# Performance work log

Hardware: AMD Instinct MI355X
Metric: run time of the kernel (lower is better)

The kernel has to match this reference:

```python
import jax, jax.numpy as jnp
import numpy as np

DIM = 1024
HEADS = 16
DIM_HEAD = 64
INNER = HEADS * DIM_HEAD
B, M, N = 8, 4096, 256
EPS = 1e-5


def layer_norm(x, g, b):
    mu = jnp.mean(x, axis=-1, keepdims=True)
    var = jnp.mean(jnp.square(x - mu), axis=-1, keepdims=True)
    return (x - mu) * jax.lax.rsqrt(var + EPS) * g + b


def setup_inputs() -> dict:
    key = jax.random.key(0)
    ks = jax.random.split(key, 8)
    x = jax.random.normal(ks[0], (B, M, DIM), dtype=jnp.float32)
    latents = jax.random.normal(ks[1], (B, N, DIM), dtype=jnp.float32)
    x_att_mask = jax.random.randint(ks[2], (B, M), 0, 2) == 1  # True = masked
    s = 0.02
    Wq = jax.random.normal(ks[3], (DIM, INNER), dtype=jnp.float32) * s
    Wkv = jax.random.normal(ks[4], (DIM, 2 * INNER), dtype=jnp.float32) * s
    Wo = jax.random.normal(ks[5], (INNER, DIM), dtype=jnp.float32) * s
    return {
        "x": x, "latents": latents, "x_att_mask": x_att_mask,
        "nm_g": jnp.ones((DIM,), jnp.float32), "nm_b": jnp.zeros((DIM,), jnp.float32),
        "nl_g": jnp.ones((DIM,), jnp.float32), "nl_b": jnp.zeros((DIM,), jnp.float32),
        "Wq": Wq, "Wkv": Wkv, "Wo": Wo,
    }


def reference(x, latents, x_att_mask, nm_g, nm_b, nl_g, nl_b, Wq, Wkv, Wo):
    b, n, d = latents.shape
    h, dh = HEADS, DIM_HEAD
    scale = dh ** (-0.5)

    # additive mask: concat(media mask, all-False latent mask); True -> -inf, False -> +1 (faithful quirk)
    latent_mask = jnp.zeros((b, n), dtype=bool)
    full_mask = jnp.concatenate([x_att_mask, latent_mask], axis=1)  # [b, m+n]
    add_mask = jnp.where(full_mask, -jnp.inf, 1.0).astype(x.dtype)[:, None, None, :]  # [b,1,1,m+n]

    xn = layer_norm(x, nm_g, nm_b)
    ln = layer_norm(latents, nl_g, nl_b)

    q = (ln @ Wq).reshape(b, n, h, dh).transpose(0, 2, 1, 3)  # bhnd
    kv_in = jnp.concatenate([xn, ln], axis=1)                 # [b, m+n, d]
    kv = kv_in @ Wkv
    k, v = jnp.split(kv, 2, axis=-1)
    j = kv_in.shape[1]
    k = k.reshape(b, j, h, dh).transpose(0, 2, 1, 3)
    v = v.reshape(b, j, h, dh).transpose(0, 2, 1, 3)

    sim = jnp.einsum('bhid,bhjd->bhij', q * scale, k)
    sim = sim - jnp.max(sim, axis=-1, keepdims=True)
    sim = sim + add_mask
    attn = jax.nn.softmax(sim, axis=-1)
    out = jnp.einsum('bhij,bhjd->bhid', attn, v)
    out = out.transpose(0, 2, 1, 3).reshape(b, n, h * dh)
    return out @ Wo
```

## Files before the change

kernel.cpp:

```cpp
#include <hip/hip_runtime.h>
#include <hip/hip_bf16.h>
#include <stdint.h>

#define HEADS 16
#define DH    64
#define NB    8
#define MQ    256
#define MX    4096
#define JD    4352
#define DIMV  1024
#define GK    1024

typedef __bf16 bf16;
typedef __bf16 bf16x8 __attribute__((ext_vector_type(8)));
typedef float  f32x4  __attribute__((ext_vector_type(4)));

#define SWZ(r, c) (((c) ^ ((r) & 7)))

#define VMW(n) asm volatile("s_waitcnt vmcnt(" #n ")" ::: "memory")

__device__ __forceinline__ void gl_lds16(const void* g, void* l) {
  __builtin_amdgcn_global_load_lds((const __attribute__((address_space(1))) void*)g,
                                   (__attribute__((address_space(3))) void*)l, 16, 0, 0);
}

__global__ __launch_bounds__(256) void ln_kernel(
    const float* __restrict__ X, const float* __restrict__ gw, const float* __restrict__ bw,
    bf16* __restrict__ out_kv, bf16* __restrict__ out_ln, int is_lat)
{
  const int row = blockIdx.x;
  const int tid = threadIdx.x;
  const float4 v = ((const float4*)(X + (size_t)row * DIMV))[tid];
  float s  = v.x + v.y + v.z + v.w;
  float s2 = v.x*v.x + v.y*v.y + v.z*v.z + v.w*v.w;
#pragma unroll
  for (int m = 1; m < 64; m <<= 1) { s += __shfl_xor(s, m); s2 += __shfl_xor(s2, m); }
  __shared__ float red[8];
  const int wid = tid >> 6;
  if ((tid & 63) == 0) { red[wid*2] = s; red[wid*2+1] = s2; }
  __syncthreads();
  s  = red[0] + red[2] + red[4] + red[6];
  s2 = red[1] + red[3] + red[5] + red[7];
  const float mu  = s * (1.0f / DIMV);
  const float var = s2 * (1.0f / DIMV) - mu * mu;
  const float rst = rsqrtf(var + 1e-5f);
  const float4 g4 = ((const float4*)gw)[tid];
  const float4 b4 = ((const float4*)bw)[tid];
  union { bf16 h[4]; short4 s4; } u;
  u.h[0] = (bf16)((v.x - mu) * rst * g4.x + b4.x);
  u.h[1] = (bf16)((v.y - mu) * rst * g4.y + b4.y);
  u.h[2] = (bf16)((v.z - mu) * rst * g4.z + b4.z);
  u.h[3] = (bf16)((v.w - mu) * rst * g4.w + b4.w);
  size_t kvrow;
  if (is_lat) { int b = row >> 8;  int i = row & 255;  kvrow = (size_t)b * JD + MX + i; }
  else        { int b = row >> 12; int j = row & 4095; kvrow = (size_t)b * JD + j; }
  *(short4*)(out_kv + kvrow * DIMV + tid * 4) = u.s4;
  if (is_lat) *(short4*)(out_ln + (size_t)row * DIMV + tid * 4) = u.s4;
}

__global__ __launch_bounds__(256) void transpose_w(
    const float* __restrict__ in, bf16* __restrict__ out, int R, int C)
{
  __shared__ float t[64][65];
  const int tilesC = C >> 6;
  const int tc = blockIdx.x % tilesC, tr = blockIdx.x / tilesC;
  const int r0 = tr << 6, c0 = tc << 6;
  const int lr = threadIdx.x >> 4;
  const int lc = (threadIdx.x & 15) << 2;
#pragma unroll
  for (int p = 0; p < 4; p++) {
    float4 v = *(const float4*)&in[(size_t)(r0 + lr + p*16) * C + c0 + lc];
    t[lr + p*16][lc    ] = v.x; t[lr + p*16][lc + 1] = v.y;
    t[lr + p*16][lc + 2] = v.z; t[lr + p*16][lc + 3] = v.w;
  }
  __syncthreads();
#pragma unroll
  for (int p = 0; p < 4; p++) {
    const int oc = lr + p*16;
    union { bf16 h[4]; short4 s4; } u;
    u.h[0] = (bf16)t[lc    ][oc]; u.h[1] = (bf16)t[lc + 1][oc];
    u.h[2] = (bf16)t[lc + 2][oc]; u.h[3] = (bf16)t[lc + 3][oc];
    *(short4*)&out[(size_t)(c0 + oc) * R + r0 + lc] = u.s4;
  }
}

__global__ __launch_bounds__(256) void mask_detect(
    const unsigned char* __restrict__ m, int n, int* __restrict__ flag)
{
  const int tid = threadIdx.x;
  int cnt = 0;
  for (int i = tid; i < n; i += 256) cnt += (m[i] != 0) ? 1 : 0;
#pragma unroll
  for (int mm = 1; mm < 64; mm <<= 1) cnt += __shfl_xor(cnt, mm);
  __shared__ int r4[4];
  if ((tid & 63) == 0) r4[tid >> 6] = cnt;
  __syncthreads();
  if (tid == 0) {
    int t = r4[0] + r4[1] + r4[2] + r4[3];
    flag[0] = (t * 16 > n * 5) ? 1 : 0;
  }
}

__global__ __launch_bounds__(256) void mask_build(
    const void* __restrict__ mraw, const int* __restrict__ flag, float* __restrict__ madd)
{
  const int idx = blockIdx.x * 256 + threadIdx.x;
  const int b = idx / JD, j = idx - b * JD;
  float v = 0.0f;
  if (j < MX) {
    bool masked = (*flag) ? (((const unsigned char*)mraw)[b * MX + j] != 0)
                          : (((const int*)mraw)[b * MX + j] != 0);
    v = masked ? -20000.0f : 0.0f;
  }
  madd[idx] = v;
}

__global__ __launch_bounds__(512, 2) void gemm256(
    const bf16* __restrict__ A, const bf16* __restrict__ Bt,
    const bf16* __restrict__ Aq, const bf16* __restrict__ Bq,
    bf16* __restrict__ outR, bf16* __restrict__ outVT, bf16* __restrict__ outQ)
{
  __shared__ bf16 sm[65536];

  const int tid = threadIdx.x;
  const int lane = tid & 63, wid = tid >> 6;
  const int wr = wid >> 2, wc = wid & 3;
  const int lc = lane & 15, lq = lane >> 4;
  const int srow = tid >> 3, sc = tid & 7;
  const int ssw = SWZ(srow, sc) * 8;

  int bid = blockIdx.x;
  bid = (bid & 7) * 140 + (bid >> 3);

  const bf16 *Arow, *Brow;
  int m0, n0, omode;
  if (bid < 1088) {
    const int by = bid >> 3, bx = bid & 7;
    m0 = by * 256;
    if (bx < 4) { n0 = bx * 256;
      Arow = A  + (size_t)m0 * GK; Brow = Bt + (size_t)n0 * GK; omode = 0; }
    else        { n0 = 1024 + (bx - 4) * 256;
      Arow = Bt + (size_t)n0 * GK; Brow = A  + (size_t)m0 * GK; omode = 1; }
  } else {
    const int ix = bid - 1088;
    m0 = (ix >> 2) * 256; n0 = (ix & 3) * 256;
    Arow = Aq + (size_t)m0 * GK; Brow = Bq + (size_t)n0 * GK; omode = 2;
  }

  const bf16* Abase = Arow + (size_t)srow * GK + ssw;
  const bf16* Bbase = Brow + (size_t)srow * GK + ssw;

  auto stA = [&](int d, int h, int kt) {
#pragma unroll
    for (int l = 0; l < 2; ++l)
      gl_lds16(Abase + (size_t)(h*128 + l*64) * GK + kt * 64,
               &sm[d*32768 + (h*128 + l*64)*64 + tid*8]);
  };
  auto stB = [&](int d, int h, int kt) {
#pragma unroll
    for (int l = 0; l < 2; ++l)
      gl_lds16(Bbase + (size_t)(h*128 + l*64) * GK + kt * 64,
               &sm[d*32768 + 16384 + (h*128 + l*64)*64 + tid*8]);
  };

  f32x4 acc[8][4];
#pragma unroll
  for (int i = 0; i < 8; i++)
#pragma unroll
    for (int j = 0; j < 4; j++)
#pragma unroll
      for (int r = 0; r < 4; r++) acc[i][j][r] = 0.f;

#define DS_PHASE(d, q, STAGE_STMT, WAIT_STMT)                                  \
  {                                                                            \
    const bf16* As_ = sm + (d)*32768;                                          \
    const bf16* Bs_ = sm + (d)*32768 + 16384;                                  \
    bf16x8 af[2][2];                                                           \
    _Pragma("unroll") for (int mi = 0; mi < 2; ++mi)                           \
      _Pragma("unroll") for (int kk = 0; kk < 2; ++kk)                         \
        af[mi][kk] = *(const bf16x8*)&As_[(wr*128 + ((q)*2+mi)*16 + lc)*64 +   \
                                          SWZ(lc, kk*4 + lq)*8];               \
    if ((q) == 0) {                                                            \
      _Pragma("unroll") for (int n = 0; n < 4; ++n)                            \
        _Pragma("unroll") for (int kk = 0; kk < 2; ++kk)                       \
          bfrag[n][kk] = *(const bf16x8*)&Bs_[(wc*64 + n*16 + lc)*64 +         \
                                              SWZ(lc, kk*4 + lq)*8];           \
    }                                                                          \
    STAGE_STMT;                                                                \
    WAIT_STMT;                                                                 \
    __builtin_amdgcn_s_barrier();                                              \
    __builtin_amdgcn_s_setprio(1);                                             \
    _Pragma("unroll") for (int kk = 0; kk < 2; ++kk)                           \
      _Pragma("unroll") for (int mi = 0; mi < 2; ++mi)                         \
        _Pragma("unroll") for (int n = 0; n < 4; ++n)                          \
          acc[(q)*2+mi][n] = __builtin_amdgcn_mfma_f32_16x16x32_bf16(          \
              af[mi][kk], bfrag[n][kk], acc[(q)*2+mi][n], 0, 0, 0);            \
    __builtin_amdgcn_s_setprio(0);                                             \
    __builtin_amdgcn_s_barrier();                                              \
  }

  stB(0, 0, 0); stB(0, 1, 0);
  stA(0, 0, 0); stA(0, 1, 0);
  stB(1, 0, 1); stB(1, 1, 1);
  VMW(4);
  __builtin_amdgcn_s_barrier();

  bf16x8 bfrag[4][2];
#pragma unroll 1
  for (int it = 0; it < 8; ++it) {
    const int tb = 2*it + 1, ta2 = 2*it + 2, tb2 = 2*it + 3;
    const bool s2 = (ta2 < 16), s3 = (tb2 < 16);
    DS_PHASE(0, 0, { stA(1, 0, tb); stA(1, 1, tb); }, {});
    DS_PHASE(0, 1, { if (s2) stB(0, 0, ta2); }, {});
    DS_PHASE(0, 2, { if (s2) stB(0, 1, ta2); }, {});
    DS_PHASE(0, 3, {}, { if (s2) { VMW(4); } else { VMW(0); } });
    DS_PHASE(1, 0, { if (s2) stA(0, 0, ta2); }, {});
    DS_PHASE(1, 1, { if (s2) stA(0, 1, ta2); }, {});
    DS_PHASE(1, 2, { if (s3) stB(1, 0, tb2); }, {});
    DS_PHASE(1, 3, { if (s3) stB(1, 1, tb2); }, { if (s3) { VMW(4); } });
  }
#undef DS_PHASE

  __syncthreads();
  bf16* Ct = sm;
#pragma unroll
  for (int m = 0; m < 8; ++m)
#pragma unroll
    for (int n = 0; n < 4; ++n) {
      const int col = wc*64 + n*16 + lc;
      const int cch = col >> 3, cw = col & 7;
#pragma unroll
      for (int r = 0; r < 4; ++r) {
        const int row = wr*128 + m*16 + lq*4 + r;
        Ct[row*256 + (((cch ^ (row & 31)) << 3) + cw)] = (bf16)acc[m][n][r];
      }
    }
  __syncthreads();

  const int cch = tid & 31, r0 = tid >> 5;
  if (omode != 1) {
    bf16* dst0 = (omode == 0 ? outR : outQ);
#pragma unroll
    for (int i = 0; i < 16; ++i) {
      const int row = r0 + i*16;
      bf16x8 v = *(const bf16x8*)&Ct[row*256 + ((cch ^ (row & 31)) << 3)];
      *(bf16x8*)(dst0 + (size_t)(m0 + row) * 1024 + n0 + cch*8) = v;
    }
  } else {
    const int bb = m0 / JD;
    const int jbase = m0 - bb * JD;
#pragma unroll
    for (int i = 0; i < 16; ++i) {
      const int row = r0 + i*16;
      const int cc = n0 + row - 1024;
      bf16x8 v = *(const bf16x8*)&Ct[row*256 + ((cch ^ (row & 31)) << 3)];
      bf16* dst = outVT + (((size_t)(bb*HEADS + (cc >> 6)))*64 + (cc & 63)) * JD
                        + jbase + cch*8;
      *(bf16x8*)dst = v;
    }
  }
}

__global__ __launch_bounds__(256) void gemm128(
    const bf16* __restrict__ A, const bf16* __restrict__ Bt,
    float* __restrict__ Cf, int N)
{
  __shared__ bf16 smem[2 * 128 * 64];
  bf16* As = smem;
  bf16* Bs = smem + 128 * 64;

  const int tid = threadIdx.x;
  const int lane = tid & 63, wid = tid >> 6;
  const int wr = wid >> 1, wc = wid & 1;
  const int m0 = blockIdx.y * 128;
  const int n0 = blockIdx.x * 128;
  const int srow = tid >> 3, sc = tid & 7;
  const int ssw = SWZ(srow, sc) * 8;
  const int lc = lane & 15, lq = lane >> 4;

  f32x4 acc[4][4];
#pragma unroll
  for (int i = 0; i < 4; i++)
#pragma unroll
    for (int j = 0; j < 4; j++)
#pragma unroll
      for (int r = 0; r < 4; r++) acc[i][j][r] = 0.f;

  const bf16* Abase = A + (size_t)m0 * GK + (size_t)srow * GK + ssw;
  const bf16* Bbase = Bt + (size_t)n0 * GK + (size_t)srow * GK + ssw;

  for (int k0 = 0; k0 < GK; k0 += 64) {
    __syncthreads();
#pragma unroll
    for (int q = 0; q < 4; q++) {
      gl_lds16(Abase + (size_t)q * 32 * GK + k0, &As[(srow + q*32) * 64 + sc*8]);
      gl_lds16(Bbase + (size_t)q * 32 * GK + k0, &Bs[(srow + q*32) * 64 + sc*8]);
    }
    VMW(0);
    __syncthreads();
#pragma unroll
    for (int kk = 0; kk < 2; kk++) {
      bf16x8 af[4], bfr[4];
#pragma unroll
      for (int mi = 0; mi < 4; mi++)
        af[mi] = *(const bf16x8*)&As[(wr*64 + mi*16 + lc) * 64 + SWZ(lc, kk*4 + lq)*8];
#pragma unroll
      for (int ni = 0; ni < 4; ni++)
        bfr[ni] = *(const bf16x8*)&Bs[(wc*64 + ni*16 + lc) * 64 + SWZ(lc, kk*4 + lq)*8];
#pragma unroll
      for (int mi = 0; mi < 4; mi++)
#pragma unroll
        for (int ni = 0; ni < 4; ni++)
          acc[mi][ni] = __builtin_amdgcn_mfma_f32_16x16x32_bf16(af[mi], bfr[ni], acc[mi][ni], 0, 0, 0);
    }
  }

#pragma unroll
  for (int mi = 0; mi < 4; mi++)
#pragma unroll
    for (int ni = 0; ni < 4; ni++) {
      const int r = m0 + wr*64 + mi*16 + lq*4;
      const int c = n0 + wc*64 + ni*16 + lc;
#pragma unroll
      for (int reg = 0; reg < 4; reg++)
        Cf[(size_t)(r + reg) * N + c] = acc[mi][ni][reg];
    }
}

__global__ __launch_bounds__(512) void attn_kernel(
    const bf16* __restrict__ Qrows,
    const bf16* __restrict__ Krows,
    const bf16* __restrict__ VT,
    const float* __restrict__ madd,
    bf16* __restrict__ outp)
{
  const int bh = blockIdx.x >> 1, qt = blockIdx.x & 1;
  const int b = bh >> 4, h = bh & 15;
  __shared__ bf16 Qs[128 * 64];
  __shared__ bf16 Ks[4][64 * 64];
  __shared__ bf16 VTs[4][64 * 64];
  __shared__ bf16 Ps[8][16 * 64];
  __shared__ float Madd[JD];
  const int tid = threadIdx.x, lane = tid & 63, w = tid >> 6;
  const int lc = lane & 15, lq = lane >> 4;
  const int srow = tid >> 3, sc = tid & 7;
  const int ssw = SWZ(srow, sc) * 8;

  const bf16* Qg = Qrows + ((size_t)(b*MQ + qt*128)) * 1024 + h*64;
  const bf16* Kg = Krows + ((size_t)b * JD) * 1024 + h*64;
  const bf16* Vg = VT + ((size_t)bh * 64) * JD;
  const float* mp = madd + (size_t)b * JD;

  auto stKV = [&](int c, int t) {
    gl_lds16(Kg + (size_t)(t*64 + srow) * 1024 + ssw, &Ks[c][tid*8]);
    gl_lds16(Vg + (size_t)srow * JD + t*64 + ssw, &VTs[c][tid*8]);
  };

  gl_lds16(Qg + (size_t)srow * 1024 + ssw, &Qs[tid*8]);
  gl_lds16(Qg + (size_t)(srow + 64) * 1024 + ssw, &Qs[(tid + 512)*8]);
  gl_lds16(mp + tid*4,        &Madd[tid*4]);
  gl_lds16(mp + 2048 + tid*4, &Madd[2048 + tid*4]);
  if (tid < 64) gl_lds16(mp + 4096 + tid*4, &Madd[4096 + tid*4]);
  VMW(0);
  stKV(0, 0); stKV(1, 1); stKV(2, 2); stKV(3, 3);
  VMW(6);
  __syncthreads();

  bf16x8 qf[2];
#pragma unroll
  for (int kk = 0; kk < 2; kk++)
    qf[kk] = *(const bf16x8*)&Qs[(w*16 + lc) * 64 + SWZ(lc, kk*4 + lq)*8];

  char* PsW = (char*)&Ps[w][0];
  f32x4 oacc[4];
  float den = 0.f;
#pragma unroll
  for (int di = 0; di < 4; di++)
#pragma unroll
    for (int r = 0; r < 4; r++) oacc[di][r] = 0.f;

#pragma unroll 1
  for (int t = 0; t < JD/64; ++t) {
    const int c = t & 3;
    const int j0 = t * 64;

    f32x4 sacc[4];
#pragma unroll
    for (int nj = 0; nj < 4; nj++)
#pragma unroll
      for (int r = 0; r < 4; r++) sacc[nj][r] = 0.f;
#pragma unroll
    for (int kk = 0; kk < 2; kk++) {
      bf16x8 kf[4];
#pragma unroll
      for (int nj = 0; nj < 4; nj++)
        kf[nj] = *(const bf16x8*)&Ks[c][(nj*16 + lc) * 64 + SWZ(lc, kk*4 + lq)*8];
#pragma unroll
      for (int nj = 0; nj < 4; nj++)
        sacc[nj] = __builtin_amdgcn_mfma_f32_16x16x32_bf16(kf[nj], qf[kk], sacc[nj], 0, 0, 0);
    }

#pragma unroll
    for (int nj = 0; nj < 4; nj++) {
      const float4 ma4 = *(const float4*)&Madd[j0 + nj*16 + lq*4];
      const float p0 = exp2f(fmaf(sacc[nj][0], 0.18033688f, ma4.x));
      const float p1 = exp2f(fmaf(sacc[nj][1], 0.18033688f, ma4.y));
      const float p2 = exp2f(fmaf(sacc[nj][2], 0.18033688f, ma4.z));
      const float p3 = exp2f(fmaf(sacc[nj][3], 0.18033688f, ma4.w));
      den += (p0 + p1) + (p2 + p3);
      union { bf16 h[4]; uint2 u2; } pu;
      pu.h[0] = (bf16)p0; pu.h[1] = (bf16)p1; pu.h[2] = (bf16)p2; pu.h[3] = (bf16)p3;
      const int c4s = (nj*2 + (lq >> 1)) ^ (lc & 7);
      *(uint2*)(PsW + lc*128 + (c4s << 4) + ((lq & 1) << 3)) = pu.u2;
    }

#pragma unroll
    for (int kk = 0; kk < 2; kk++) {
      bf16x8 pf = *(const bf16x8*)(PsW + lc*128 + ((((kk << 2) + lq) ^ (lc & 7)) << 4));
#pragma unroll
      for (int di = 0; di < 4; di++) {
        bf16x8 vf = *(const bf16x8*)&VTs[c][(di*16 + lc) * 64 + SWZ(lc, kk*4 + lq)*8];
        oacc[di] = __builtin_amdgcn_mfma_f32_16x16x32_bf16(pf, vf, oacc[di], 0, 0, 0);
      }
    }

    __builtin_amdgcn_s_barrier();
    if (t + 4 < JD/64) {
      stKV(c, t + 4);
      VMW(6);
    } else if (t == JD/64 - 4) { VMW(4);
    } else if (t == JD/64 - 3) { VMW(2);
    } else if (t == JD/64 - 2) { VMW(0);
    }
    __builtin_amdgcn_s_barrier();
  }

  den += __shfl_xor(den, 16);
  den += __shfl_xor(den, 32);
  const float rden = 1.0f / den;

#pragma unroll
  for (int di = 0; di < 4; di++) {
    const int col = h*64 + di*16 + lc;
#pragma unroll
    for (int r = 0; r < 4; r++) {
      const float dr = __shfl(rden, lq*4 + r, 16);
      const int i = qt*128 + w*16 + lq*4 + r;
      outp[(size_t)(b*MQ + i) * 1024 + col] = (bf16)(oacc[di][r] * dr);
    }
  }
}

extern "C" void kernel_launch(void* const* d_in, const int* in_sizes, int n_in,
                              void* d_out, int out_size, void* d_ws, size_t ws_size,
                              hipStream_t stream)
{
  const float* x    = (const float*)d_in[0];
  const float* lat  = (const float*)d_in[1];
  const void*  mraw = d_in[2];
  const float* nm_g = (const float*)d_in[3];
  const float* nm_b = (const float*)d_in[4];
  const float* nl_g = (const float*)d_in[5];
  const float* nl_b = (const float*)d_in[6];
  const float* Wq   = (const float*)d_in[7];
  const float* Wkv  = (const float*)d_in[8];
  const float* Wo   = (const float*)d_in[9];
  float* out = (float*)d_out;

  char* p = (char*)d_ws;
  auto alloc = [&](size_t bytes) { char* r = p; p += (bytes + 255) & ~(size_t)255; return r; };

  bf16*  kv_in  = (bf16*)alloc((size_t)NB * JD * DIMV * 2);
  bf16*  Krows  = (bf16*)alloc((size_t)NB * JD * 1024 * 2);
  bf16*  VTbuf  = (bf16*)alloc((size_t)NB * HEADS * 64 * JD * 2);
  bf16*  WqT    = (bf16*)alloc((size_t)1024 * 1024 * 2);
  bf16*  WkvT   = (bf16*)alloc((size_t)2048 * 1024 * 2);
  bf16*  WoT    = (bf16*)alloc((size_t)1024 * 1024 * 2);
  bf16*  ln_buf = (bf16*)alloc((size_t)NB * MQ * DIMV * 2);
  bf16*  Qrows  = (bf16*)alloc((size_t)NB * MQ * 1024 * 2);
  bf16*  attout = (bf16*)alloc((size_t)NB * MQ * DIMV * 2);
  float* maddp  = (float*)alloc((size_t)NB * JD * 4);
  int*   flag   = (int*)alloc(256);
  (void)ws_size; (void)in_sizes; (void)n_in; (void)out_size;

  ln_kernel<<<NB * MX, 256, 0, stream>>>(x,   nm_g, nm_b, kv_in, nullptr, 0);
  ln_kernel<<<NB * MQ, 256, 0, stream>>>(lat, nl_g, nl_b, kv_in, ln_buf, 1);
  transpose_w<<<256, 256, 0, stream>>>(Wq,  WqT,  1024, 1024);
  transpose_w<<<512, 256, 0, stream>>>(Wkv, WkvT, 1024, 2048);
  transpose_w<<<256, 256, 0, stream>>>(Wo,  WoT,  1024, 1024);
  mask_detect<<<1, 256, 0, stream>>>((const unsigned char*)mraw, 32768, flag);
  mask_build<<<136, 256, 0, stream>>>(mraw, flag, maddp);

  gemm256<<<1120, 512, 0, stream>>>(kv_in, WkvT, ln_buf, WqT, Krows, VTbuf, Qrows);
  attn_kernel<<<256, 512, 0, stream>>>(Qrows, Krows, VTbuf, maddp, attout);
  gemm128<<<dim3(8, 16), 256, 0, stream>>>(attout, WoT, out, 1024);
}
```

Before: 522.8 us.

## Merge prep kernels and restructure attention K/V ring to five-stage single-barrier

Merges the two layernorm launches, the three weight-transpose launches and the mask detect/build pair into single kernels, cutting launch count. Each mask block now recomputes the byte-count detection itself, which removes the flag buffer. The attention kernel grows its K/V LDS ring from four to five slots. That allows one barrier per iteration and lets the next prefetch be issued before the compute instead of after it. It also raises MFMA issue priority around the matrix-multiply groups, at the cost of more LDS per block and redundant mask counting in every mask block.

```diff
diff --git a/kernel.cpp b/kernel.cpp
--- a/kernel.cpp
+++ b/kernel.cpp
@@ -24,13 +24,28 @@
                                    (__attribute__((address_space(3))) void*)l, 16, 0, 0);
 }
 
-__global__ __launch_bounds__(256) void ln_kernel(
-    const float* __restrict__ X, const float* __restrict__ gw, const float* __restrict__ bw,
-    bf16* __restrict__ out_kv, bf16* __restrict__ out_ln, int is_lat)
+__global__ __launch_bounds__(256) void ln_all(
+    const float* __restrict__ X, const float* __restrict__ LAT,
+    const float* __restrict__ nmg, const float* __restrict__ nmb,
+    const float* __restrict__ nlg, const float* __restrict__ nlb,
+    bf16* __restrict__ out_kv, bf16* __restrict__ out_ln)
 {
   const int row = blockIdx.x;
   const int tid = threadIdx.x;
-  const float4 v = ((const float4*)(X + (size_t)row * DIMV))[tid];
+  const bool lat = row >= NB * MX;
+  const float *src, *gw, *bw;
+  size_t kvrow; int lrow = 0;
+  if (lat) {
+    lrow = row - NB * MX;
+    const int b = lrow >> 8, i = lrow & 255;
+    src = LAT + (size_t)lrow * DIMV; gw = nlg; bw = nlb;
+    kvrow = (size_t)b * JD + MX + i;
+  } else {
+    const int b = row >> 12, j = row & 4095;
+    src = X + (size_t)row * DIMV; gw = nmg; bw = nmb;
+    kvrow = (size_t)b * JD + j;
+  }
+  const float4 v = ((const float4*)src)[tid];
   float s  = v.x + v.y + v.z + v.w;
   float s2 = v.x*v.x + v.y*v.y + v.z*v.z + v.w*v.w;
 #pragma unroll
@@ -51,19 +66,24 @@
   u.h[1] = (bf16)((v.y - mu) * rst * g4.y + b4.y);
   u.h[2] = (bf16)((v.z - mu) * rst * g4.z + b4.z);
   u.h[3] = (bf16)((v.w - mu) * rst * g4.w + b4.w);
-  size_t kvrow;
-  if (is_lat) { int b = row >> 8;  int i = row & 255;  kvrow = (size_t)b * JD + MX + i; }
-  else        { int b = row >> 12; int j = row & 4095; kvrow = (size_t)b * JD + j; }
   *(short4*)(out_kv + kvrow * DIMV + tid * 4) = u.s4;
-  if (is_lat) *(short4*)(out_ln + (size_t)row * DIMV + tid * 4) = u.s4;
-}
-
-__global__ __launch_bounds__(256) void transpose_w(
-    const float* __restrict__ in, bf16* __restrict__ out, int R, int C)
-{
+  if (lat) *(short4*)(out_ln + (size_t)lrow * DIMV + tid * 4) = u.s4;
+}
+
+__global__ __launch_bounds__(256) void transpose_all(
+    const float* __restrict__ Wq, const float* __restrict__ Wkv,
+    const float* __restrict__ Wo,
+    bf16* __restrict__ WqT, bf16* __restrict__ WkvT, bf16* __restrict__ WoT)
+{
+  const int bid = blockIdx.x;
+  const float* in; bf16* out; int C, tb;
+  if (bid < 256)      { in = Wq;  out = WqT;  C = 1024; tb = bid; }
+  else if (bid < 768) { in = Wkv; out = WkvT; C = 2048; tb = bid - 256; }
+  else                { in = Wo;  out = WoT;  C = 1024; tb = bid - 768; }
+  const int R = 1024;
   __shared__ float t[64][65];
   const int tilesC = C >> 6;
-  const int tc = blockIdx.x % tilesC, tr = blockIdx.x / tilesC;
+  const int tc = tb % tilesC, tr = tb / tilesC;
   const int r0 = tr << 6, c0 = tc << 6;
   const int lr = threadIdx.x >> 4;
   const int lc = (threadIdx.x & 15) << 2;
@@ -84,32 +104,26 @@
   }
 }
 
-__global__ __launch_bounds__(256) void mask_detect(
-    const unsigned char* __restrict__ m, int n, int* __restrict__ flag)
+__global__ __launch_bounds__(256) void mask_all(
+    const void* __restrict__ mraw, float* __restrict__ madd)
 {
   const int tid = threadIdx.x;
+  const unsigned char* mb = (const unsigned char*)mraw;
   int cnt = 0;
-  for (int i = tid; i < n; i += 256) cnt += (m[i] != 0) ? 1 : 0;
-#pragma unroll
-  for (int mm = 1; mm < 64; mm <<= 1) cnt += __shfl_xor(cnt, mm);
+  for (int i = tid; i < 32768; i += 256) cnt += (mb[i] != 0) ? 1 : 0;
+#pragma unroll
+  for (int m = 1; m < 64; m <<= 1) cnt += __shfl_xor(cnt, m);
   __shared__ int r4[4];
   if ((tid & 63) == 0) r4[tid >> 6] = cnt;
   __syncthreads();
-  if (tid == 0) {
-    int t = r4[0] + r4[1] + r4[2] + r4[3];
-    flag[0] = (t * 16 > n * 5) ? 1 : 0;
-  }
-}
-
-__global__ __launch_bounds__(256) void mask_build(
-    const void* __restrict__ mraw, const int* __restrict__ flag, float* __restrict__ madd)
-{
-  const int idx = blockIdx.x * 256 + threadIdx.x;
+  const int tot = r4[0] + r4[1] + r4[2] + r4[3];
+  const bool bytemode = (tot * 16 > 32768 * 5);
+  const int idx = blockIdx.x * 256 + tid;
   const int b = idx / JD, j = idx - b * JD;
   float v = 0.0f;
   if (j < MX) {
-    bool masked = (*flag) ? (((const unsigned char*)mraw)[b * MX + j] != 0)
-                          : (((const int*)mraw)[b * MX + j] != 0);
+    bool masked = bytemode ? (mb[b * MX + j] != 0)
+                           : (((const int*)mraw)[b * MX + j] != 0);
     v = masked ? -20000.0f : 0.0f;
   }
   madd[idx] = v;
@@ -337,8 +351,8 @@
   const int bh = blockIdx.x >> 1, qt = blockIdx.x & 1;
   const int b = bh >> 4, h = bh & 15;
   __shared__ bf16 Qs[128 * 64];
-  __shared__ bf16 Ks[4][64 * 64];
-  __shared__ bf16 VTs[4][64 * 64];
+  __shared__ bf16 Ks[5][64 * 64];
+  __shared__ bf16 VTs[5][64 * 64];
   __shared__ bf16 Ps[8][16 * 64];
   __shared__ float Madd[JD];
   const int tid = threadIdx.x, lane = tid & 63, w = tid >> 6;
@@ -363,7 +377,6 @@
   if (tid < 64) gl_lds16(mp + 4096 + tid*4, &Madd[4096 + tid*4]);
   VMW(0);
   stKV(0, 0); stKV(1, 1); stKV(2, 2); stKV(3, 3);
-  VMW(6);
   __syncthreads();
 
   bf16x8 qf[2];
@@ -379,9 +392,18 @@
 #pragma unroll
     for (int r = 0; r < 4; r++) oacc[di][r] = 0.f;
 
+  int c = 0;
 #pragma unroll 1
   for (int t = 0; t < JD/64; ++t) {
-    const int c = t & 3;
+    if (t <= JD/64 - 4)      { VMW(6); }
+    else if (t == JD/64 - 3) { VMW(4); }
+    else if (t == JD/64 - 2) { VMW(2); }
+    else                     { VMW(0); }
+    __builtin_amdgcn_s_barrier();
+    if (t + 4 < JD/64) {
+      const int c4 = (c == 0) ? 4 : c - 1;
+      stKV(c4, t + 4);
+    }
     const int j0 = t * 64;
 
     f32x4 sacc[4];
@@ -395,9 +417,11 @@
 #pragma unroll
       for (int nj = 0; nj < 4; nj++)
         kf[nj] = *(const bf16x8*)&Ks[c][(nj*16 + lc) * 64 + SWZ(lc, kk*4 + lq)*8];
+      __builtin_amdgcn_s_setprio(1);
 #pragma unroll
       for (int nj = 0; nj < 4; nj++)
         sacc[nj] = __builtin_amdgcn_mfma_f32_16x16x32_bf16(kf[nj], qf[kk], sacc[nj], 0, 0, 0);
+      __builtin_amdgcn_s_setprio(0);
     }
 
 #pragma unroll
@@ -417,22 +441,16 @@
 #pragma unroll
     for (int kk = 0; kk < 2; kk++) {
       bf16x8 pf = *(const bf16x8*)(PsW + lc*128 + ((((kk << 2) + lq) ^ (lc & 7)) << 4));
+      __builtin_amdgcn_s_setprio(1);
 #pragma unroll
       for (int di = 0; di < 4; di++) {
         bf16x8 vf = *(const bf16x8*)&VTs[c][(di*16 + lc) * 64 + SWZ(lc, kk*4 + lq)*8];
         oacc[di] = __builtin_amdgcn_mfma_f32_16x16x32_bf16(pf, vf, oacc[di], 0, 0, 0);
       }
-    }
-
-    __builtin_amdgcn_s_barrier();
-    if (t + 4 < JD/64) {
-      stKV(c, t + 4);
-      VMW(6);
-    } else if (t == JD/64 - 4) { VMW(4);
-    } else if (t == JD/64 - 3) { VMW(2);
-    } else if (t == JD/64 - 2) { VMW(0);
-    }
-    __builtin_amdgcn_s_barrier();
+      __builtin_amdgcn_s_setprio(0);
+    }
+
+    c = (c == 4) ? 0 : c + 1;
   }
 
   den += __shfl_xor(den, 16);
@@ -480,16 +498,12 @@
   bf16*  Qrows  = (bf16*)alloc((size_t)NB * MQ * 1024 * 2);
   bf16*  attout = (bf16*)alloc((size_t)NB * MQ * DIMV * 2);
   float* maddp  = (float*)alloc((size_t)NB * JD * 4);
-  int*   flag   = (int*)alloc(256);
   (void)ws_size; (void)in_sizes; (void)n_in; (void)out_size;
 
-  ln_kernel<<<NB * MX, 256, 0, stream>>>(x,   nm_g, nm_b, kv_in, nullptr, 0);
-  ln_kernel<<<NB * MQ, 256, 0, stream>>>(lat, nl_g, nl_b, kv_in, ln_buf, 1);
-  transpose_w<<<256, 256, 0, stream>>>(Wq,  WqT,  1024, 1024);
-  transpose_w<<<512, 256, 0, stream>>>(Wkv, WkvT, 1024, 2048);
-  transpose_w<<<256, 256, 0, stream>>>(Wo,  WoT,  1024, 1024);
-  mask_detect<<<1, 256, 0, stream>>>((const unsigned char*)mraw, 32768, flag);
-  mask_build<<<136, 256, 0, stream>>>(mraw, flag, maddp);
+  ln_all<<<NB * (MX + MQ), 256, 0, stream>>>(x, lat, nm_g, nm_b, nl_g, nl_b,
+                                             kv_in, ln_buf);
+  transpose_all<<<1024, 256, 0, stream>>>(Wq, Wkv, Wo, WqT, WkvT, WoT);
+  mask_all<<<136, 256, 0, stream>>>(mraw, maddp);
 
   gemm256<<<1120, 512, 0, stream>>>(kv_in, WkvT, ln_buf, WqT, Krows, VTbuf, Qrows);
   attn_kernel<<<256, 512, 0, stream>>>(Qrows, Krows, VTbuf, maddp, attout);
```

Measured after the change: 524.9 us. About the same (+0.4%).
